# Optimization experiments

Hardware: AMD Instinct MI355X
Metric: run time of the kernel (lower is better)

## Reference

```python
import jax, jax.numpy as jnp
import numpy as np

IMAGE = 224; P = 16; G = 14; N = 196; C = 3; PD = 768
DIM = 512; DEPTH = 4; H = 8; DH = 64; INNER = 512; MLP = 2048
SCALE = DIM ** -0.5
EPS = 1e-5


def layernorm(x, g, b):
    m = x.mean(-1, keepdims=True)
    v = ((x - m) ** 2).mean(-1, keepdims=True)
    return (x - m) * jax.lax.rsqrt(v + EPS) * g + b


def compute_embedding(W, coords):
    # W: (DIM//2, 2), coords: (b, p, 2) -> (b, p, DIM)
    proj = jnp.einsum('od,bpd->bpo', W, coords)
    s = (2.0 / (DIM // 2)) ** 0.5
    return jnp.concatenate([s * jnp.cos(proj), s * jnp.sin(proj)], axis=-1)


def setup_inputs():
    key = jax.random.key(0)
    ks = jax.random.split(key, 8)
    B = 64
    img = jax.random.normal(ks[0], (B, C, IMAGE, IMAGE), jnp.float32)
    noise_token = jax.random.normal(ks[1], (B, DIM), jnp.float32)
    A_noise = jax.random.normal(ks[2], (B, 2, 2), jnp.float32)
    b_noise = jax.random.normal(ks[3], (B, 2), jnp.float32)
    m, n = np.meshgrid(np.arange(G), np.arange(G))
    X = jnp.asarray(np.reshape(np.stack((m, n), -1), (-1, 2)), jnp.float32)  # (N,2)
    Wfreq = jax.random.normal(ks[4], (DIM // 2, 2), jnp.float32)  # band_width=1.0
    base_pos = compute_embedding(Wfreq, X[None])  # (1,N,DIM), trainable param
    A_mean = jnp.eye(2, dtype=jnp.float32)
    b_mean = jnp.zeros((2,), jnp.float32)
    A_std = jnp.zeros((2, 2), jnp.float32)  # variance_init = 0.0
    b_std = jnp.zeros((2,), jnp.float32)

    def lin(k, i, o):
        return jax.random.normal(k, (i, o), jnp.float32) / np.float32(np.sqrt(i))

    Wpe = lin(ks[5], PD, DIM); bpe = jnp.zeros((DIM,), jnp.float32)
    Wep = lin(ks[6], DIM, PD); bep = jnp.zeros((PD,), jnp.float32)
    kk = jax.random.split(ks[7], DEPTH * 4)
    Wqkv = jnp.stack([lin(kk[4 * i + 0], DIM, 3 * INNER) for i in range(DEPTH)])
    Wout = jnp.stack([lin(kk[4 * i + 1], INNER, DIM) for i in range(DEPTH)])
    bout = jnp.zeros((DEPTH, DIM), jnp.float32)
    Wff1 = jnp.stack([lin(kk[4 * i + 2], DIM, MLP) for i in range(DEPTH)])
    bff1 = jnp.zeros((DEPTH, MLP), jnp.float32)
    Wff2 = jnp.stack([lin(kk[4 * i + 3], MLP, DIM) for i in range(DEPTH)])
    bff2 = jnp.zeros((DEPTH, DIM), jnp.float32)
    ln1_g = jnp.ones((DEPTH, DIM), jnp.float32); ln1_b = jnp.zeros((DEPTH, DIM), jnp.float32)
    ln2_g = jnp.ones((DEPTH, DIM), jnp.float32); ln2_b = jnp.zeros((DEPTH, DIM), jnp.float32)
    return dict(img=img, noise_token=noise_token, A_noise=A_noise, b_noise=b_noise,
                Wfreq=Wfreq, X=X, base_pos=base_pos,
                A_mean=A_mean, b_mean=b_mean, A_std=A_std, b_std=b_std,
                Wpe=Wpe, bpe=bpe, Wep=Wep, bep=bep,
                ln1_g=ln1_g, ln1_b=ln1_b, Wqkv=Wqkv, Wout=Wout, bout=bout,
                ln2_g=ln2_g, ln2_b=ln2_b, Wff1=Wff1, bff1=bff1, Wff2=Wff2, bff2=bff2)


def reference(img, noise_token, A_noise, b_noise, Wfreq, X, base_pos,
              A_mean, b_mean, A_std, b_std, Wpe, bpe, Wep, bep,
              ln1_g, ln1_b, Wqkv, Wout, bout, ln2_g, ln2_b, Wff1, bff1, Wff2, bff2):
    del noise_token  # deleted in original forward
    B = img.shape[0]
    # patchify: b c (h p1) (w p2) -> b (h w) (p1 p2 c)
    x = img.reshape(B, C, G, P, G, P).transpose(0, 2, 4, 3, 5, 1).reshape(B, N, PD)
    x = x @ Wpe + bpe  # patch_to_embedding
    # transformed positional embedding (_compute_transformed_embedding)
    A = A_mean + jax.nn.softplus(A_std) * A_noise          # (B,2,2)
    bvec = b_mean + jax.nn.softplus(b_std) * b_noise       # (B,2)
    X_t = jnp.einsum('pd,bdo->bpo', X, A) + bvec[:, None, :]
    pos = compute_embedding(Wfreq, X_t)                    # (B,N,DIM)
    # pos-only attention scores: identical across layers and heads
    dots = jnp.einsum('bid,jd->bij', pos, base_pos[0]) * SCALE
    attn = jax.nn.softmax(dots, axis=-1)                   # (B,N,N)
    for l in range(DEPTH):
        # PreNorm(SplitAttention) -- note: NO residual around attention
        xn = layernorm(x, ln1_g[l], ln1_b[l])
        qkv = xn @ Wqkv[l]
        v = qkv[..., 2 * INNER:].reshape(B, N, H, DH).transpose(0, 2, 1, 3)  # b h n d
        out = jnp.einsum('bij,bhjd->bhid', attn, v)
        out = out.transpose(0, 2, 1, 3).reshape(B, N, INNER)
        x = out @ Wout[l] + bout[l]
        # Residual(PreNorm(FeedForward))
        xn2 = layernorm(x, ln2_g[l], ln2_b[l])
        ff = jax.nn.gelu(xn2 @ Wff1[l] + bff1[l], approximate=False) @ Wff2[l] + bff2[l]
        x = ff + x
    x = x @ Wep + bep  # embedding_to_patch
    # unpatchify: b (h w) (p1 p2 c) -> b c (h p1) (w p2)
    return x.reshape(B, G, G, P, P, C).transpose(0, 5, 1, 3, 2, 4).reshape(B, C, IMAGE, IMAGE)
```

## Files before the change

### kernel.cpp

```cpp
#include <hip/hip_runtime.h>
#include <hip/hip_bf16.h>
#include <math.h>


#define B_    64
#define NTOK  196
#define CCH   3
#define PDIM  768
#define DIM   512
#define MLP   2048
#define MROWS (B_ * NTOK)
#define IMGHW 224
#define KPAD  224
#define VTLD  (B_ * KPAD)

typedef __attribute__((ext_vector_type(8))) short bf16x8;
typedef __attribute__((ext_vector_type(4))) float f32x4;

static __device__ __forceinline__ unsigned short f2b(float f) {
    unsigned int x = __float_as_uint(f);
    unsigned int r = (x + 0x7FFFu + ((x >> 16) & 1u)) >> 16;
    return (unsigned short)r;
}
static __device__ __forceinline__ float softplusf(float x) {
    return fmaxf(x, 0.0f) + log1pf(expf(-fabsf(x)));
}

__global__ __launch_bounds__(256) void patchify_kernel(const float* __restrict__ img,
                                                       unsigned short* __restrict__ xp) {
    long idx = (long)blockIdx.x * blockDim.x + threadIdx.x;
    if (idx >= (long)MROWS * PDIM) return;
    int pd = (int)(idx % PDIM);
    long bn = idx / PDIM;
    int n = (int)(bn % NTOK);
    int b = (int)(bn / NTOK);
    int c = pd % 3;
    int p12 = pd / 3;
    int p1 = p12 >> 4, p2 = p12 & 15;
    int g1 = n / 14, g2 = n % 14;
    long src = (((long)b * CCH + c) * IMGHW + (g1 * 16 + p1)) * IMGHW + (g2 * 16 + p2);
    xp[idx] = f2b(img[src]);
}

__global__ __launch_bounds__(256) void unpatchify_kernel(const float* __restrict__ y,
                                                         float* __restrict__ out) {
    long idx = (long)blockIdx.x * blockDim.x + threadIdx.x;
    if (idx >= (long)B_ * CCH * IMGHW * IMGHW) return;
    int ww = (int)(idx % IMGHW);
    long r = idx / IMGHW;
    int hh = (int)(r % IMGHW);
    r /= IMGHW;
    int c = (int)(r % CCH);
    int b = (int)(r / CCH);
    int g1 = hh >> 4, p1 = hh & 15;
    int g2 = ww >> 4, p2 = ww & 15;
    int n = g1 * 14 + g2;
    int pd = (p1 * 16 + p2) * 3 + c;
    out[idx] = y[((long)b * NTOK + n) * PDIM + pd];
}

__global__ __launch_bounds__(256) void pos_kernel(const float* __restrict__ Xc,
                                                  const float* __restrict__ Wfreq,
                                                  const float* __restrict__ A_noise,
                                                  const float* __restrict__ b_noise,
                                                  const float* __restrict__ A_mean,
                                                  const float* __restrict__ b_mean,
                                                  const float* __restrict__ A_std,
                                                  const float* __restrict__ b_std,
                                                  unsigned short* __restrict__ pos) {
    int bp = blockIdx.x;
    int b = bp / NTOK, p = bp % NTOK;
    int o = threadIdx.x;
    float a00 = A_mean[0] + softplusf(A_std[0]) * A_noise[b * 4 + 0];
    float a01 = A_mean[1] + softplusf(A_std[1]) * A_noise[b * 4 + 1];
    float a10 = A_mean[2] + softplusf(A_std[2]) * A_noise[b * 4 + 2];
    float a11 = A_mean[3] + softplusf(A_std[3]) * A_noise[b * 4 + 3];
    float bv0 = b_mean[0] + softplusf(b_std[0]) * b_noise[b * 2 + 0];
    float bv1 = b_mean[1] + softplusf(b_std[1]) * b_noise[b * 2 + 1];
    float x0 = Xc[p * 2 + 0], x1 = Xc[p * 2 + 1];
    float xt0 = x0 * a00 + x1 * a10 + bv0;
    float xt1 = x0 * a01 + x1 * a11 + bv1;
    float proj = Wfreq[o * 2 + 0] * xt0 + Wfreq[o * 2 + 1] * xt1;
    float sv, cv;
    sincosf(proj, &sv, &cv);
    const float s = 0.08838834764831843f;
    pos[(long)bp * DIM + o]       = f2b(s * cv);
    pos[(long)bp * DIM + 256 + o] = f2b(s * sv);
}

__global__ __launch_bounds__(64) void softmax_kernel(const float* __restrict__ dots,
                                                     unsigned short* __restrict__ attn) {
    long row = blockIdx.x;
    const float* p = dots + row * NTOK;
    unsigned short* q = attn + row * NTOK;
    int t = threadIdx.x;
    float v[4];
    float mx = -INFINITY;
    #pragma unroll
    for (int j = 0; j < 4; j++) {
        int i = t + j * 64;
        v[j] = (i < NTOK) ? p[i] : -INFINITY;
        mx = fmaxf(mx, v[j]);
    }
    #pragma unroll
    for (int off = 32; off >= 1; off >>= 1) mx = fmaxf(mx, __shfl_xor(mx, off));
    float sum = 0.f;
    #pragma unroll
    for (int j = 0; j < 4; j++) {
        int i = t + j * 64;
        v[j] = (i < NTOK) ? expf(v[j] - mx) : 0.f;
        sum += v[j];
    }
    #pragma unroll
    for (int off = 32; off >= 1; off >>= 1) sum += __shfl_xor(sum, off);
    float inv = 1.0f / sum;
    #pragma unroll
    for (int j = 0; j < 4; j++) {
        int i = t + j * 64;
        if (i < NTOK) q[i] = f2b(v[j] * inv);
    }
}

__global__ __launch_bounds__(128) void ln_kernel(const float* __restrict__ x,
                                                 const float* __restrict__ g,
                                                 const float* __restrict__ bb,
                                                 unsigned short* __restrict__ out) {
    long row = blockIdx.x;
    int t = threadIdx.x;
    float4 v = *(const float4*)(x + row * DIM + t * 4);
    float s = v.x + v.y + v.z + v.w;
    float q = v.x * v.x + v.y * v.y + v.z * v.z + v.w * v.w;
    #pragma unroll
    for (int off = 32; off >= 1; off >>= 1) {
        s += __shfl_xor(s, off);
        q += __shfl_xor(q, off);
    }
    __shared__ float red[4];
    int lane = t & 63, wv = t >> 6;
    if (lane == 0) { red[wv * 2] = s; red[wv * 2 + 1] = q; }
    __syncthreads();
    float S = red[0] + red[2], Q = red[1] + red[3];
    float mean = S * (1.0f / DIM);
    float var = Q * (1.0f / DIM) - mean * mean;
    float rs = rsqrtf(var + 1e-5f);
    float4 gg = *(const float4*)(g + t * 4);
    float4 bv = *(const float4*)(bb + t * 4);
    ushort4 o;
    o.x = f2b((v.x - mean) * rs * gg.x + bv.x);
    o.y = f2b((v.y - mean) * rs * gg.y + bv.y);
    o.z = f2b((v.z - mean) * rs * gg.z + bv.z);
    o.w = f2b((v.w - mean) * rs * gg.w + bv.w);
    *(ushort4*)(out + row * DIM + t * 4) = o;
}

struct TDesc {
    const float* in;
    unsigned short* out;
    int R, C, ld, cb, bbase, tx, trans;
};
struct TPack { TDesc d[19]; int n; };

__global__ __launch_bounds__(256) void wconv_kernel(TPack p) {
    __shared__ float t[32][33];
    int bid = blockIdx.x;
    int di = 0;
    for (int i = 1; i < p.n; ++i) if (bid >= p.d[i].bbase) di = i;
    TDesc d = p.d[di];
    int local = bid - d.bbase;
    int bx = local % d.tx, by = local / d.tx;
    int r0 = by * 32, c0 = bx * 32;
    int lx = threadIdx.x & 31, ly = threadIdx.x >> 5;
    if (d.trans) {
        #pragma unroll
        for (int i = 0; i < 4; i++) {
            int r = r0 + ly + i * 8, c = c0 + lx;
            t[ly + i * 8][lx] = (r < d.R && c < d.C) ? d.in[(long)r * d.ld + d.cb + c] : 0.f;
        }
        __syncthreads();
        #pragma unroll
        for (int i = 0; i < 4; i++) {
            int c = c0 + ly + i * 8, r = r0 + lx;
            if (c < d.C && r < d.R) d.out[(long)c * d.R + r] = f2b(t[lx][ly + i * 8]);
        }
    } else {
        #pragma unroll
        for (int i = 0; i < 4; i++) {
            int r = r0 + ly + i * 8, c = c0 + lx;
            if (r < d.R && c < d.C) d.out[(long)r * d.C + c] = f2b(d.in[(long)r * d.ld + d.cb + c]);
        }
    }
}

__global__ __launch_bounds__(256) void tbf16_kernel(const unsigned short* __restrict__ in,
                                                    unsigned short* __restrict__ out,
                                                    int R, int C, int inld, int outld,
                                                    int grp, int gstride) {
    __shared__ unsigned short t[32][33];
    int r0 = blockIdx.y * 32, c0 = blockIdx.x * 32;
    int lx = threadIdx.x & 31, ly = threadIdx.x >> 5;
    #pragma unroll
    for (int i = 0; i < 4; i++) {
        int r = r0 + ly + i * 8, c = c0 + lx;
        t[ly + i * 8][lx] = (r < R && c < C) ? in[(long)r * inld + c] : 0;
    }
    __syncthreads();
    #pragma unroll
    for (int i = 0; i < 4; i++) {
        int c = c0 + ly + i * 8, r = r0 + lx;
        if (c < C && r < R) {
            int oc = grp ? (r / grp) * gstride + (r % grp) : r;
            out[(long)c * outld + oc] = t[lx][ly + i * 8];
        }
    }
}

template <bool GELU, bool RESID, bool WF32, bool WB16>
__global__ __launch_bounds__(256) void mgemm(const unsigned short* __restrict__ A,
                                             const unsigned short* __restrict__ Bt,
                                             const float* __restrict__ bias,
                                             const float* __restrict__ Rsd,
                                             float* __restrict__ Cf,
                                             unsigned short* __restrict__ Cb,
                                             int M, int N, int K,
                                             int lda, int ldb, int ldc,
                                             long bsA, long bsBt, long bsC,
                                             float scale) {
    int bz = blockIdx.z;
    A  += bz * bsA;
    Bt += bz * bsBt;
    __shared__ __attribute__((aligned(16))) unsigned short As[128][40];
    __shared__ __attribute__((aligned(16))) unsigned short Bs[128][40];
    int m0 = blockIdx.y * 128, n0 = blockIdx.x * 128;
    int tid = threadIdx.x;
    int wave = tid >> 6, lane = tid & 63;
    int wm = (wave & 1) * 64, wn = (wave >> 1) * 64;
    int fr = lane & 15, fg = lane >> 4;
    int ar = tid >> 1, ah = tid & 1;

    f32x4 acc[4][4];
    #pragma unroll
    for (int i = 0; i < 4; i++)
        #pragma unroll
        for (int j = 0; j < 4; j++) acc[i][j] = (f32x4)0.f;

    int brow = n0 + ar; if (brow >= N) brow = N - 1;
    const unsigned short* pa0 = A + (long)(m0 + ar) * lda + ah * 16;
    const unsigned short* pb0 = Bt + (long)brow * ldb + ah * 16;

    for (int k0 = 0; k0 < K; k0 += 32) {
        bf16x8 a0 = *(const bf16x8*)(pa0 + k0);
        bf16x8 a1 = *(const bf16x8*)(pa0 + k0 + 8);
        bf16x8 b0 = *(const bf16x8*)(pb0 + k0);
        bf16x8 b1 = *(const bf16x8*)(pb0 + k0 + 8);
        __syncthreads();
        *(bf16x8*)&As[ar][ah * 16]     = a0;
        *(bf16x8*)&As[ar][ah * 16 + 8] = a1;
        *(bf16x8*)&Bs[ar][ah * 16]     = b0;
        *(bf16x8*)&Bs[ar][ah * 16 + 8] = b1;
        __syncthreads();
        bf16x8 af[4], bfr[4];
        #pragma unroll
        for (int i = 0; i < 4; i++) af[i]  = *(const bf16x8*)&As[wm + i * 16 + fr][fg * 8];
        #pragma unroll
        for (int j = 0; j < 4; j++) bfr[j] = *(const bf16x8*)&Bs[wn + j * 16 + fr][fg * 8];
        #pragma unroll
        for (int i = 0; i < 4; i++)
            #pragma unroll
            for (int j = 0; j < 4; j++)
                acc[i][j] = __builtin_amdgcn_mfma_f32_16x16x32_bf16(af[i], bfr[j], acc[i][j], 0, 0, 0);
    }

    long cbase = (long)bz * bsC;
    #pragma unroll
    for (int i = 0; i < 4; i++) {
        int row = m0 + wm + i * 16 + fg * 4;
        #pragma unroll
        for (int j = 0; j < 4; j++) {
            int col = n0 + wn + j * 16 + fr;
            if (col >= N) continue;
            float bv = bias ? bias[col] : 0.f;
            #pragma unroll
            for (int r = 0; r < 4; r++) {
                float v = acc[i][j][r] * scale + bv;
                if (GELU) v = 0.5f * v * (1.0f + erff(v * 0.70710678118654752f));
                long ci = cbase + (long)(row + r) * ldc + col;
                if (RESID) v += Rsd[ci];
                if (WF32) Cf[ci] = v;
                if (WB16) Cb[ci] = f2b(v);
            }
        }
    }
}


extern "C" void kernel_launch(void* const* d_in, const int* in_sizes, int n_in,
                              void* d_out, int out_size, void* d_ws, size_t ws_size,
                              hipStream_t stream) {
    const float* img      = (const float*)d_in[0];
    const float* A_noise  = (const float*)d_in[2];
    const float* b_noise  = (const float*)d_in[3];
    const float* Wfreq    = (const float*)d_in[4];
    const float* Xc       = (const float*)d_in[5];
    const float* base_pos = (const float*)d_in[6];
    const float* A_mean   = (const float*)d_in[7];
    const float* b_mean   = (const float*)d_in[8];
    const float* A_std    = (const float*)d_in[9];
    const float* b_std    = (const float*)d_in[10];
    const float* Wpe      = (const float*)d_in[11];
    const float* bpe      = (const float*)d_in[12];
    const float* Wep      = (const float*)d_in[13];
    const float* bep      = (const float*)d_in[14];
    const float* ln1_g    = (const float*)d_in[15];
    const float* ln1_b    = (const float*)d_in[16];
    const float* Wqkv     = (const float*)d_in[17];
    const float* Wout     = (const float*)d_in[18];
    const float* bout     = (const float*)d_in[19];
    const float* ln2_g    = (const float*)d_in[20];
    const float* ln2_b    = (const float*)d_in[21];
    const float* Wff1     = (const float*)d_in[22];
    const float* bff1     = (const float*)d_in[23];
    const float* Wff2     = (const float*)d_in[24];
    const float* bff2     = (const float*)d_in[25];

    char* ws = (char*)d_ws;
    float*          x_f    = (float*)(ws + 0);
    unsigned short* sb0    = (unsigned short*)(ws + 25690112);
    unsigned short* attn16 = (unsigned short*)(ws + 38535168);
    unsigned short* v16    = (unsigned short*)(ws + 43452928);
    unsigned short* vT     = (unsigned short*)(ws + 56297984);
    unsigned short* outT   = (unsigned short*)(ws + 70978048);
    unsigned short* h1     = (unsigned short*)(ws + 83823104);
    unsigned short* pat16  = (unsigned short*)(ws + 83823104);
    unsigned short* pos16  = (unsigned short*)(ws + 83823104 + 19267584);
    float*          dots   = (float*)(ws + 83823104 + 19267584 + 12845056);
    float*          y_f    = (float*)(ws + 83823104);
    char* wp = ws + 135203328;
    unsigned short* WpeT   = (unsigned short*)(wp);
    unsigned short* WqkvT  = (unsigned short*)(wp + 786432);
    unsigned short* WoutT  = (unsigned short*)(wp + 786432 + 2097152);
    unsigned short* Wff1T  = (unsigned short*)(wp + 786432 + 2 * 2097152);
    unsigned short* Wff2T  = (unsigned short*)(wp + 786432 + 2 * 2097152 + 8388608);
    unsigned short* WepT   = (unsigned short*)(wp + 786432 + 2 * 2097152 + 2 * 8388608);
    unsigned short* bp16   = (unsigned short*)(wp + 2 * 786432 + 2 * 2097152 + 2 * 8388608);

    const float SCALE = 0.044194173824159216f;

    hipMemsetAsync(vT, 0, (size_t)512 * VTLD * 2, stream);

    {
        TPack p; int bb = 0, di = 0;
        auto add = [&](const float* in, unsigned short* out, int R, int C, int ld, int cb, int tr) {
            TDesc d; d.in = in; d.out = out; d.R = R; d.C = C; d.ld = ld; d.cb = cb;
            d.trans = tr; d.tx = (C + 31) / 32; d.bbase = bb;
            bb += d.tx * ((R + 31) / 32);
            p.d[di++] = d;
        };
        add(Wpe, WpeT, 768, 512, 512, 0, 1);
        for (int l = 0; l < 4; l++) add(Wqkv + (long)l * 512 * 1536, WqkvT + (long)l * 512 * 512, 512, 512, 1536, 1024, 1);
        for (int l = 0; l < 4; l++) add(Wout + (long)l * 512 * 512, WoutT + (long)l * 512 * 512, 512, 512, 512, 0, 1);
        for (int l = 0; l < 4; l++) add(Wff1 + (long)l * 512 * 2048, Wff1T + (long)l * 2048 * 512, 512, 2048, 2048, 0, 1);
        for (int l = 0; l < 4; l++) add(Wff2 + (long)l * 2048 * 512, Wff2T + (long)l * 512 * 2048, 2048, 512, 512, 0, 1);
        add(Wep, WepT, 512, 768, 768, 0, 1);
        add(base_pos, bp16, 196, 512, 512, 0, 0);
        p.n = di;
        wconv_kernel<<<dim3(bb), dim3(256), 0, stream>>>(p);
    }

    patchify_kernel<<<dim3((MROWS * PDIM + 255) / 256), dim3(256), 0, stream>>>(img, pat16);
    mgemm<false, false, true, false><<<dim3(4, 98), dim3(256), 0, stream>>>(
        pat16, WpeT, bpe, nullptr, x_f, nullptr, MROWS, DIM, PDIM, PDIM, PDIM, DIM, 0, 0, 0, 1.0f);
    pos_kernel<<<dim3(MROWS), dim3(256), 0, stream>>>(
        Xc, Wfreq, A_noise, b_noise, A_mean, b_mean, A_std, b_std, pos16);
    mgemm<false, false, true, false><<<dim3(2, 98), dim3(256), 0, stream>>>(
        pos16, bp16, nullptr, nullptr, dots, nullptr, MROWS, NTOK, DIM, DIM, DIM, NTOK, 0, 0, 0, SCALE);
    softmax_kernel<<<dim3(MROWS), dim3(64), 0, stream>>>(dots, attn16);

    for (int l = 0; l < 4; l++) {
        ln_kernel<<<dim3(MROWS), dim3(128), 0, stream>>>(x_f, ln1_g + l * DIM, ln1_b + l * DIM, sb0);
        mgemm<false, false, false, true><<<dim3(4, 98), dim3(256), 0, stream>>>(
            sb0, WqkvT + (long)l * 512 * 512, nullptr, nullptr, nullptr, v16,
            MROWS, DIM, DIM, DIM, DIM, DIM, 0, 0, 0, 1.0f);
        tbf16_kernel<<<dim3(16, 392), dim3(256), 0, stream>>>(v16, vT, MROWS, DIM, DIM, VTLD, NTOK, KPAD);
        mgemm<false, false, false, true><<<dim3(2, 4, B_), dim3(256), 0, stream>>>(
            vT, attn16, nullptr, nullptr, nullptr, outT,
            512, NTOK, KPAD, VTLD, NTOK, MROWS, KPAD, (long)NTOK * NTOK, NTOK, 1.0f);
        tbf16_kernel<<<dim3(392, 16), dim3(256), 0, stream>>>(outT, sb0, DIM, MROWS, MROWS, DIM, 0, 0);
        mgemm<false, false, true, false><<<dim3(4, 98), dim3(256), 0, stream>>>(
            sb0, WoutT + (long)l * 512 * 512, bout + l * DIM, nullptr, x_f, nullptr,
            MROWS, DIM, DIM, DIM, DIM, DIM, 0, 0, 0, 1.0f);
        ln_kernel<<<dim3(MROWS), dim3(128), 0, stream>>>(x_f, ln2_g + l * DIM, ln2_b + l * DIM, sb0);
        mgemm<true, false, false, true><<<dim3(16, 98), dim3(256), 0, stream>>>(
            sb0, Wff1T + (long)l * 2048 * 512, bff1 + l * MLP, nullptr, nullptr, h1,
            MROWS, MLP, DIM, DIM, DIM, MLP, 0, 0, 0, 1.0f);
        mgemm<false, true, true, true><<<dim3(4, 98), dim3(256), 0, stream>>>(
            h1, Wff2T + (long)l * 512 * 2048, bff2 + l * DIM, x_f, x_f, outT,
            MROWS, DIM, MLP, MLP, MLP, DIM, 0, 0, 0, 1.0f);
    }

    mgemm<false, false, true, false><<<dim3(6, 98), dim3(256), 0, stream>>>(
        outT, WepT, bep, nullptr, y_f, nullptr, MROWS, PDIM, DIM, DIM, DIM, PDIM, 0, 0, 0, 1.0f);
    unpatchify_kernel<<<dim3(((long)B_ * CCH * IMGHW * IMGHW + 255) / 256), dim3(256), 0, stream>>>(
        y_f, (float*)d_out);
}
```

Measured before the change: 1.334 ms.

## Use direct global-to-LDS loads in GEMM and drop transpose kernels in attention

Result: slower. 1.637 ms (+22.7%).

```diff
diff --git a/kernel.cpp b/kernel.cpp
--- a/kernel.cpp
+++ b/kernel.cpp
@@ -24,6 +24,12 @@
 }
 static __device__ __forceinline__ float softplusf(float x) {
     return fmaxf(x, 0.0f) + log1pf(expf(-fabsf(x)));
+}
+
+typedef const __attribute__((address_space(1))) unsigned int* gp1_t;
+typedef __attribute__((address_space(3))) unsigned int* lp3_t;
+static __device__ __forceinline__ void gld16(const unsigned short* g, unsigned short* l) {
+    __builtin_amdgcn_global_load_lds((gp1_t)g, (lp3_t)l, 16, 0, 0);
 }
 
 __global__ __launch_bounds__(256) void patchify_kernel(const float* __restrict__ img,
@@ -92,7 +98,7 @@
                                                      unsigned short* __restrict__ attn) {
     long row = blockIdx.x;
     const float* p = dots + row * NTOK;
-    unsigned short* q = attn + row * NTOK;
+    unsigned short* q = attn + row * KPAD;
     int t = threadIdx.x;
     float v[4];
     float mx = -INFINITY;
@@ -118,6 +124,7 @@
     for (int j = 0; j < 4; j++) {
         int i = t + j * 64;
         if (i < NTOK) q[i] = f2b(v[j] * inv);
+        else if (i < KPAD) q[i] = 0;
     }
 }
 
@@ -191,29 +198,6 @@
     }
 }
 
-__global__ __launch_bounds__(256) void tbf16_kernel(const unsigned short* __restrict__ in,
-                                                    unsigned short* __restrict__ out,
-                                                    int R, int C, int inld, int outld,
-                                                    int grp, int gstride) {
-    __shared__ unsigned short t[32][33];
-    int r0 = blockIdx.y * 32, c0 = blockIdx.x * 32;
-    int lx = threadIdx.x & 31, ly = threadIdx.x >> 5;
-    #pragma unroll
-    for (int i = 0; i < 4; i++) {
-        int r = r0 + ly + i * 8, c = c0 + lx;
-        t[ly + i * 8][lx] = (r < R && c < C) ? in[(long)r * inld + c] : 0;
-    }
-    __syncthreads();
-    #pragma unroll
-    for (int i = 0; i < 4; i++) {
-        int c = c0 + ly + i * 8, r = r0 + lx;
-        if (c < C && r < R) {
-            int oc = grp ? (r / grp) * gstride + (r % grp) : r;
-            out[(long)c * outld + oc] = t[lx][ly + i * 8];
-        }
-    }
-}
-
 template <bool GELU, bool RESID, bool WF32, bool WB16>
 __global__ __launch_bounds__(256) void mgemm(const unsigned short* __restrict__ A,
                                              const unsigned short* __restrict__ Bt,
@@ -224,18 +208,34 @@
                                              int M, int N, int K,
                                              int lda, int ldb, int ldc,
                                              long bsA, long bsBt, long bsC,
-                                             float scale) {
+                                             float scale, int grp, int gstride) {
     int bz = blockIdx.z;
     A  += bz * bsA;
     Bt += bz * bsBt;
-    __shared__ __attribute__((aligned(16))) unsigned short As[128][40];
-    __shared__ __attribute__((aligned(16))) unsigned short Bs[128][40];
+    __shared__ __attribute__((aligned(1024))) unsigned short As[4096];
+    __shared__ __attribute__((aligned(1024))) unsigned short Bs[4096];
     int m0 = blockIdx.y * 128, n0 = blockIdx.x * 128;
     int tid = threadIdx.x;
     int wave = tid >> 6, lane = tid & 63;
     int wm = (wave & 1) * 64, wn = (wave >> 1) * 64;
     int fr = lane & 15, fg = lane >> 4;
-    int ar = tid >> 1, ah = tid & 1;
+
+    int g1 = wave * 64 + lane;
+    int g2 = g1 + 256;
+    int f1 = g1 >> 7, r1 = g1 & 127;
+    int f2 = g2 >> 7, r2 = g2 & 127;
+    int ra1 = m0 + r1; if (ra1 > M - 1) ra1 = M - 1;
+    int ra2 = m0 + r2; if (ra2 > M - 1) ra2 = M - 1;
+    int rb1 = n0 + r1; if (rb1 > N - 1) rb1 = N - 1;
+    int rb2 = n0 + r2; if (rb2 > N - 1) rb2 = N - 1;
+    const unsigned short* pa1 = A + (long)ra1 * lda + f1 * 8;
+    const unsigned short* pa2 = A + (long)ra2 * lda + f2 * 8;
+    const unsigned short* pb1 = Bt + (long)rb1 * ldb + f1 * 8;
+    const unsigned short* pb2 = Bt + (long)rb2 * ldb + f2 * 8;
+    unsigned short* lA1 = &As[wave * 512];
+    unsigned short* lA2 = &As[wave * 512 + 2048];
+    unsigned short* lB1 = &Bs[wave * 512];
+    unsigned short* lB2 = &Bs[wave * 512 + 2048];
 
     f32x4 acc[4][4];
     #pragma unroll
@@ -243,26 +243,20 @@
         #pragma unroll
         for (int j = 0; j < 4; j++) acc[i][j] = (f32x4)0.f;
 
-    int brow = n0 + ar; if (brow >= N) brow = N - 1;
-    const unsigned short* pa0 = A + (long)(m0 + ar) * lda + ah * 16;
-    const unsigned short* pb0 = Bt + (long)brow * ldb + ah * 16;
-
     for (int k0 = 0; k0 < K; k0 += 32) {
-        bf16x8 a0 = *(const bf16x8*)(pa0 + k0);
-        bf16x8 a1 = *(const bf16x8*)(pa0 + k0 + 8);
-        bf16x8 b0 = *(const bf16x8*)(pb0 + k0);
-        bf16x8 b1 = *(const bf16x8*)(pb0 + k0 + 8);
         __syncthreads();
-        *(bf16x8*)&As[ar][ah * 16]     = a0;
-        *(bf16x8*)&As[ar][ah * 16 + 8] = a1;
-        *(bf16x8*)&Bs[ar][ah * 16]     = b0;
-        *(bf16x8*)&Bs[ar][ah * 16 + 8] = b1;
+        gld16(pa1 + k0, lA1);
+        gld16(pa2 + k0, lA2);
+        gld16(pb1 + k0, lB1);
+        gld16(pb2 + k0, lB2);
         __syncthreads();
         bf16x8 af[4], bfr[4];
         #pragma unroll
-        for (int i = 0; i < 4; i++) af[i]  = *(const bf16x8*)&As[wm + i * 16 + fr][fg * 8];
-        #pragma unroll
-        for (int j = 0; j < 4; j++) bfr[j] = *(const bf16x8*)&Bs[wn + j * 16 + fr][fg * 8];
+        for (int i = 0; i < 4; i++)
+            af[i]  = *(const bf16x8*)&As[(fg * 128 + wm + i * 16 + fr) * 8];
+        #pragma unroll
+        for (int j = 0; j < 4; j++)
+            bfr[j] = *(const bf16x8*)&Bs[(fg * 128 + wn + j * 16 + fr) * 8];
         #pragma unroll
         for (int i = 0; i < 4; i++)
             #pragma unroll
@@ -278,12 +272,14 @@
         for (int j = 0; j < 4; j++) {
             int col = n0 + wn + j * 16 + fr;
             if (col >= N) continue;
+            int ocol = (grp > 0) ? ((col / grp) * gstride + (col % grp)) : col;
             float bv = bias ? bias[col] : 0.f;
             #pragma unroll
             for (int r = 0; r < 4; r++) {
+                if (row + r >= M) continue;
                 float v = acc[i][j][r] * scale + bv;
                 if (GELU) v = 0.5f * v * (1.0f + erff(v * 0.70710678118654752f));
-                long ci = cbase + (long)(row + r) * ldc + col;
+                long ci = cbase + (long)(row + r) * ldc + ocol;
                 if (RESID) v += Rsd[ci];
                 if (WF32) Cf[ci] = v;
                 if (WB16) Cb[ci] = f2b(v);
@@ -326,22 +322,21 @@
     float*          x_f    = (float*)(ws + 0);
     unsigned short* sb0    = (unsigned short*)(ws + 25690112);
     unsigned short* attn16 = (unsigned short*)(ws + 38535168);
-    unsigned short* v16    = (unsigned short*)(ws + 43452928);
-    unsigned short* vT     = (unsigned short*)(ws + 56297984);
-    unsigned short* outT   = (unsigned short*)(ws + 70978048);
-    unsigned short* h1     = (unsigned short*)(ws + 83823104);
-    unsigned short* pat16  = (unsigned short*)(ws + 83823104);
-    unsigned short* pos16  = (unsigned short*)(ws + 83823104 + 19267584);
-    float*          dots   = (float*)(ws + 83823104 + 19267584 + 12845056);
-    float*          y_f    = (float*)(ws + 83823104);
-    char* wp = ws + 135203328;
+    unsigned short* vT     = (unsigned short*)(ws + 44154880);
+    unsigned short* xb16   = (unsigned short*)(ws + 58834944);
+    unsigned short* h1     = (unsigned short*)(ws + 71680000);
+    unsigned short* pat16  = (unsigned short*)(ws + 71680000);
+    unsigned short* pos16  = (unsigned short*)(ws + 90947584);
+    float*          dots   = (float*)(ws + 103792640);
+    float*          y_f    = (float*)(ws + 71680000);
+    char* wp = ws + 123060224;
     unsigned short* WpeT   = (unsigned short*)(wp);
     unsigned short* WqkvT  = (unsigned short*)(wp + 786432);
-    unsigned short* WoutT  = (unsigned short*)(wp + 786432 + 2097152);
-    unsigned short* Wff1T  = (unsigned short*)(wp + 786432 + 2 * 2097152);
-    unsigned short* Wff2T  = (unsigned short*)(wp + 786432 + 2 * 2097152 + 8388608);
-    unsigned short* WepT   = (unsigned short*)(wp + 786432 + 2 * 2097152 + 2 * 8388608);
-    unsigned short* bp16   = (unsigned short*)(wp + 2 * 786432 + 2 * 2097152 + 2 * 8388608);
+    unsigned short* WoutT  = (unsigned short*)(wp + 2883584);
+    unsigned short* Wff1T  = (unsigned short*)(wp + 4980736);
+    unsigned short* Wff2T  = (unsigned short*)(wp + 13369344);
+    unsigned short* WepT   = (unsigned short*)(wp + 21757952);
+    unsigned short* bp16   = (unsigned short*)(wp + 22544384);
 
     const float SCALE = 0.044194173824159216f;
 
@@ -368,37 +363,39 @@
 
     patchify_kernel<<<dim3((MROWS * PDIM + 255) / 256), dim3(256), 0, stream>>>(img, pat16);
     mgemm<false, false, true, false><<<dim3(4, 98), dim3(256), 0, stream>>>(
-        pat16, WpeT, bpe, nullptr, x_f, nullptr, MROWS, DIM, PDIM, PDIM, PDIM, DIM, 0, 0, 0, 1.0f);
+        pat16, WpeT, bpe, nullptr, x_f, nullptr, MROWS, DIM, PDIM, PDIM, PDIM, DIM,
+        0, 0, 0, 1.0f, 0, 0);
     pos_kernel<<<dim3(MROWS), dim3(256), 0, stream>>>(
         Xc, Wfreq, A_noise, b_noise, A_mean, b_mean, A_std, b_std, pos16);
     mgemm<false, false, true, false><<<dim3(2, 98), dim3(256), 0, stream>>>(
-        pos16, bp16, nullptr, nullptr, dots, nullptr, MROWS, NTOK, DIM, DIM, DIM, NTOK, 0, 0, 0, SCALE);
+        pos16, bp16, nullptr, nullptr, dots, nullptr, MROWS, NTOK, DIM, DIM, DIM, NTOK,
+        0, 0, 0, SCALE, 0, 0);
     softmax_kernel<<<dim3(MROWS), dim3(64), 0, stream>>>(dots, attn16);
 
     for (int l = 0; l < 4; l++) {
         ln_kernel<<<dim3(MROWS), dim3(128), 0, stream>>>(x_f, ln1_g + l * DIM, ln1_b + l * DIM, sb0);
-        mgemm<false, false, false, true><<<dim3(4, 98), dim3(256), 0, stream>>>(
-            sb0, WqkvT + (long)l * 512 * 512, nullptr, nullptr, nullptr, v16,
-            MROWS, DIM, DIM, DIM, DIM, DIM, 0, 0, 0, 1.0f);
-        tbf16_kernel<<<dim3(16, 392), dim3(256), 0, stream>>>(v16, vT, MROWS, DIM, DIM, VTLD, NTOK, KPAD);
-        mgemm<false, false, false, true><<<dim3(2, 4, B_), dim3(256), 0, stream>>>(
-            vT, attn16, nullptr, nullptr, nullptr, outT,
-            512, NTOK, KPAD, VTLD, NTOK, MROWS, KPAD, (long)NTOK * NTOK, NTOK, 1.0f);
-        tbf16_kernel<<<dim3(392, 16), dim3(256), 0, stream>>>(outT, sb0, DIM, MROWS, MROWS, DIM, 0, 0);
+        mgemm<false, false, false, true><<<dim3(98, 4), dim3(256), 0, stream>>>(
+            WqkvT + (long)l * 512 * 512, sb0, nullptr, nullptr, nullptr, vT,
+            512, MROWS, DIM, DIM, DIM, VTLD, 0, 0, 0, 1.0f, NTOK, KPAD);
+        mgemm<false, false, false, true><<<dim3(4, 2, B_), dim3(256), 0, stream>>>(
+            attn16, vT, nullptr, nullptr, nullptr, sb0,
+            NTOK, DIM, KPAD, KPAD, VTLD, DIM,
+            (long)NTOK * KPAD, (long)KPAD, (long)NTOK * DIM, 1.0f, 0, 0);
         mgemm<false, false, true, false><<<dim3(4, 98), dim3(256), 0, stream>>>(
             sb0, WoutT + (long)l * 512 * 512, bout + l * DIM, nullptr, x_f, nullptr,
-            MROWS, DIM, DIM, DIM, DIM, DIM, 0, 0, 0, 1.0f);
+            MROWS, DIM, DIM, DIM, DIM, DIM, 0, 0, 0, 1.0f, 0, 0);
         ln_kernel<<<dim3(MROWS), dim3(128), 0, stream>>>(x_f, ln2_g + l * DIM, ln2_b + l * DIM, sb0);
         mgemm<true, false, false, true><<<dim3(16, 98), dim3(256), 0, stream>>>(
             sb0, Wff1T + (long)l * 2048 * 512, bff1 + l * MLP, nullptr, nullptr, h1,
-            MROWS, MLP, DIM, DIM, DIM, MLP, 0, 0, 0, 1.0f);
+            MROWS, MLP, DIM, DIM, DIM, MLP, 0, 0, 0, 1.0f, 0, 0);
         mgemm<false, true, true, true><<<dim3(4, 98), dim3(256), 0, stream>>>(
-            h1, Wff2T + (long)l * 512 * 2048, bff2 + l * DIM, x_f, x_f, outT,
-            MROWS, DIM, MLP, MLP, MLP, DIM, 0, 0, 0, 1.0f);
+            h1, Wff2T + (long)l * 512 * 2048, bff2 + l * DIM, x_f, x_f, xb16,
+            MROWS, DIM, MLP, MLP, MLP, DIM, 0, 0, 0, 1.0f, 0, 0);
     }
 
     mgemm<false, false, true, false><<<dim3(6, 98), dim3(256), 0, stream>>>(
-        outT, WepT, bep, nullptr, y_f, nullptr, MROWS, PDIM, DIM, DIM, DIM, PDIM, 0, 0, 0, 1.0f);
+        xb16, WepT, bep, nullptr, y_f, nullptr, MROWS, PDIM, DIM, DIM, DIM, PDIM,
+        0, 0, 0, 1.0f, 0, 0);
     unpatchify_kernel<<<dim3(((long)B_ * CCH * IMGHW * IMGHW + 255) / 256), dim3(256), 0, stream>>>(
         y_f, (float*)d_out);
 }
```
